# Performance work log

Hardware: AMD Instinct MI355X
Metric: run time of the kernel (lower is better)

The kernel has to match this reference:

```python
import jax, jax.numpy as jnp
import numpy as np
from jax import lax

H = W = 96
C = 3
N_PIX = H * W
N_PER_CLASS = 50   # min(size_sample_fg=100 -> shuffled to min_samples, size_sample_bg=50)
K = 5
THRESHOLD = 0.3
POS_WEIGHT = 100.0
CLEAN_THRESH = 0.6


def _sample_idx(key, valid_mask_flat, n):
    # Uniform random sample of n indices from valid positions (fixed-shape
    # replacement for tf.random.shuffle(tf.where(mask))[:n]).
    u = jax.random.uniform(key, (N_PIX,))
    score = jnp.where(valid_mask_flat, u, -1.0)
    _, idx = lax.top_k(score, n)
    return idx


def _pixel_features(img01):
    # img01: [H, W, C] in [0, 1]. Matches: reshape(img)/255 concat weighted positions.
    img_flat = img01.reshape(-1, C) / 255.0
    ii, jj = jnp.meshgrid(jnp.arange(H), jnp.arange(W), indexing='ij')
    pos = jnp.stack([ii, jj], axis=-1).reshape(-1, 2).astype(jnp.float32)
    pos = pos / jnp.array([H, W], jnp.float32) * POS_WEIGHT
    return jnp.concatenate([img_flat, pos], axis=1)  # [N_PIX, C+2]


def _process_image(img, key):
    # preprocess: (already 96x96x3) normalize & clip
    img_p = jnp.clip(img / 255.0, 0.0, 1.0)

    # extract_image_tf: clean image, pick fg/bg scribble pixels
    img_norm = img_p / jnp.max(img_p, axis=(0, 1), keepdims=True)
    cleaned = img_norm * (img_norm < CLEAN_THRESH).astype(jnp.float32)
    fg = jnp.any(cleaned > 0, axis=-1).reshape(-1)  # [N_PIX] bool
    bg = ~fg
    k_fg, k_bg = jax.random.split(key)
    fg_idx = _sample_idx(k_fg, fg, N_PER_CLASS)
    bg_idx = _sample_idx(k_bg, bg, N_PER_CLASS)

    # extract_features_tf
    feats_all = _pixel_features(img_p)                       # [N_PIX, 5]
    train_feats = jnp.concatenate([feats_all[fg_idx], feats_all[bg_idx]], axis=0)  # [100, 5]
    train_labels = jnp.concatenate([jnp.ones(N_PER_CLASS), jnp.zeros(N_PER_CLASS)])

    # segment_image_KNN_tf: standardize, brute-force cdist, top-k, label vote
    mean = jnp.mean(train_feats, axis=0)
    std = jnp.std(train_feats, axis=0)
    train_s = (train_feats - mean) / std                     # [100, 5]
    test_s = (feats_all - mean) / std                        # [N_PIX, 5]
    dist = jnp.sqrt(jnp.sum(jnp.square(test_s[:, None, :] - train_s[None, :, :]), axis=2))  # [N_PIX, 100]
    _, knn_idx = lax.top_k(-dist, K)                         # smallest-k distances
    probas = jnp.mean(train_labels[knn_idx], axis=1)         # [N_PIX]
    seg = (probas >= THRESHOLD).astype(jnp.int32).reshape(H, W)

    # mask original (preprocessed) image
    return jnp.where(seg[..., None] == 1, img_p, jnp.zeros_like(img_p))


def setup_inputs() -> dict:
    key = jax.random.key(0)
    images = jax.random.uniform(key, (32, H, W, C), dtype=jnp.float32)
    return {"images": images}


def reference(images):
    B = images.shape[0]
    keys = jax.random.split(jax.random.key(42), B)
    return jax.vmap(_process_image)(images, keys)
```

## Files before the change

### kernel.cpp

```cpp
#include <hip/hip_runtime.h>
#include <stdint.h>

#define NPIX 9216
#define NIMG 32
#define STRIP 1152

__device__ __forceinline__ uint32_t rotl32(uint32_t x, int d){ return (x<<d)|(x>>(32-d)); }

__device__ __forceinline__ void threefry(uint32_t k0, uint32_t k1, uint32_t x0, uint32_t x1,
                                         uint32_t &o0, uint32_t &o1){
  uint32_t ks2 = k0 ^ k1 ^ 0x1BD11BDAu;
  x0 += k0; x1 += k1;
  x0+=x1; x1=rotl32(x1,13); x1^=x0;
  x0+=x1; x1=rotl32(x1,15); x1^=x0;
  x0+=x1; x1=rotl32(x1,26); x1^=x0;
  x0+=x1; x1=rotl32(x1,6);  x1^=x0;
  x0+=k1; x1+=ks2+1u;
  x0+=x1; x1=rotl32(x1,17); x1^=x0;
  x0+=x1; x1=rotl32(x1,29); x1^=x0;
  x0+=x1; x1=rotl32(x1,16); x1^=x0;
  x0+=x1; x1=rotl32(x1,24); x1^=x0;
  x0+=ks2; x1+=k0+2u;
  x0+=x1; x1=rotl32(x1,13); x1^=x0;
  x0+=x1; x1=rotl32(x1,15); x1^=x0;
  x0+=x1; x1=rotl32(x1,26); x1^=x0;
  x0+=x1; x1=rotl32(x1,6);  x1^=x0;
  x0+=k0; x1+=k1+3u;
  x0+=x1; x1=rotl32(x1,17); x1^=x0;
  x0+=x1; x1=rotl32(x1,29); x1^=x0;
  x0+=x1; x1=rotl32(x1,16); x1^=x0;
  x0+=x1; x1=rotl32(x1,24); x1^=x0;
  x0+=k1; x1+=ks2+4u;
  x0+=x1; x1=rotl32(x1,13); x1^=x0;
  x0+=x1; x1=rotl32(x1,15); x1^=x0;
  x0+=x1; x1=rotl32(x1,26); x1^=x0;
  x0+=x1; x1=rotl32(x1,6);  x1^=x0;
  x0+=ks2; x1+=k0+5u;
  o0=x0; o1=x1;
}

__device__ __forceinline__ float clip01_div255(float x){
  return fminf(fmaxf(x/255.0f, 0.0f), 1.0f);
}

__global__ __launch_bounds__(256) void kmax(const float* __restrict__ in,
                                            float* __restrict__ maxpart){
  int img  = blockIdx.x / 6;
  int part = blockIdx.x % 6;
  int tid  = threadIdx.x;
  const float* base = in + (size_t)img*NPIX*3 + (size_t)part*1536*3;
  float m0=0.f, m1=0.f, m2=0.f;
#pragma unroll
  for(int k=0;k<18;k++){
    int g = k*256 + tid;
    float v = clip01_div255(base[g]);
    int c = g % 3;
    m0 = (c==0) ? fmaxf(m0,v) : m0;
    m1 = (c==1) ? fmaxf(m1,v) : m1;
    m2 = (c==2) ? fmaxf(m2,v) : m2;
  }
  for(int off=32; off>0; off>>=1){
    m0 = fmaxf(m0, __shfl_down(m0,off));
    m1 = fmaxf(m1, __shfl_down(m1,off));
    m2 = fmaxf(m2, __shfl_down(m2,off));
  }
  __shared__ float r[3][4];
  int lane = tid & 63, wv = tid >> 6;
  if(lane==0){ r[0][wv]=m0; r[1][wv]=m1; r[2][wv]=m2; }
  __syncthreads();
  if(tid==0){
    maxpart[blockIdx.x*3+0]=fmaxf(fmaxf(r[0][0],r[0][1]),fmaxf(r[0][2],r[0][3]));
    maxpart[blockIdx.x*3+1]=fmaxf(fmaxf(r[1][0],r[1][1]),fmaxf(r[1][2],r[1][3]));
    maxpart[blockIdx.x*3+2]=fmaxf(fmaxf(r[2][0],r[2][1]),fmaxf(r[2][2],r[2][3]));
  }
}

__global__ __launch_bounds__(256) void kscore(const float* __restrict__ in,
                                              const float* __restrict__ maxpart,
                                              unsigned long long* __restrict__ key50g){
#pragma clang fp contract(off)
  int b   = blockIdx.x;
  int img = b >> 4, cls = (b >> 3) & 1, sub = b & 7;
  int tid = threadIdx.x;

  __shared__ __attribute__((aligned(16))) float pixL[3456];
  __shared__ uint32_t vvL[STRIP];
  __shared__ uint64_t cand[STRIP];
  __shared__ int hist[129];
  __shared__ int ncand, bbin;

  if(tid<129) hist[tid]=0;
  if(tid==0)  ncand=0;

  const float* p = in + (size_t)img*NPIX*3;

  const float4* sp4 = (const float4*)(p + (size_t)sub*STRIP*3);
  float4* pixL4 = (float4*)pixL;
  for(int k=0;k<4;k++){ int i4=k*256+tid; if(i4<864) pixL4[i4]=sp4[i4]; }

  float c0=0.f,c1=0.f,c2=0.f;
#pragma unroll
  for(int s=0;s<6;s++){
    c0=fmaxf(c0, maxpart[(img*6+s)*3+0]);
    c1=fmaxf(c1, maxpart[(img*6+s)*3+1]);
    c2=fmaxf(c2, maxpart[(img*6+s)*3+2]);
  }

  uint32_t ik0, ik1; threefry(0u, 42u, 0u, (uint32_t)img, ik0, ik1);
  uint32_t s0, s1;   threefry(ik0, ik1, 0u, (uint32_t)cls, s0, s1);
  __syncthreads();

  for(int r=0;r<5;r++){
    int pi = tid + r*256;
    if(pi<STRIP){
      float a  = clip01_div255(pixL[pi*3+0])/c0;
      float bb = clip01_div255(pixL[pi*3+1])/c1;
      float c  = clip01_div255(pixL[pi*3+2])/c2;
      bool fg = (a>0.f && a<0.6f) || (bb>0.f && bb<0.6f) || (c>0.f && c<0.6f);
      bool valid = (cls==0) ? fg : !fg;
      uint32_t gi = (uint32_t)(sub*STRIP + pi);
      uint32_t r1,r2; threefry(s0, s1, 0u, gi, r1, r2);
      uint32_t vv = valid ? ((r1 ^ r2) >> 9) + 1u : 0u;
      vvL[pi] = vv;
      if(vv) atomicAdd(&hist[vv>>16], 1);
    }
  }
  __syncthreads();

  if(tid < 64){
    int h0 = hist[2*tid];
    int h1 = hist[2*tid+1];
    int h128 = hist[128];
    int S = h0 + h1;
    for(int off=1; off<64; off<<=1){
      int o = __shfl_down(S, off);
      if(tid + off < 64) S += o;
    }
    int ss0 = S + h128;
    int ss1 = S - h0 + h128;
    int cd = -1;
    if(ss0 >= 50) cd = 2*tid;
    if(ss1 >= 50) cd = 2*tid+1;
    if(tid==63 && h128 >= 50) cd = 128;
    for(int off=32; off>0; off>>=1){
      int o = __shfl_down(cd, off);
      cd = o > cd ? o : cd;
    }
    if(tid==0) bbin = cd;
  }
  __syncthreads();

  int bb = bbin;
  for(int r=0;r<5;r++){
    int pi = tid + r*256;
    if(pi<STRIP){
      uint32_t vv = vvL[pi];
      if((int)(vv>>16) >= bb){
        int pos = atomicAdd(&ncand,1);
        cand[pos] = ((uint64_t)vv << 14) | (uint64_t)(16383 - (sub*STRIP + pi));
      }
    }
  }
  __syncthreads();
  int m = ncand;
  for(int c=tid;c<m;c+=256){
    uint64_t k = cand[c];
    int r = 0, j = 0;
    while(j < m){
      int je = j+64 < m ? j+64 : m;
      for(; j<je; j++) r += (cand[j] > k);
      if(r >= 50) break;
    }
    if(r < 50) key50g[(size_t)b*50 + r] = k;
  }
}

__global__ __launch_bounds__(256) void kmerge(const float* __restrict__ in,
                                              const unsigned long long* __restrict__ key50g,
                                              float* __restrict__ ts2g,
                                              float* __restrict__ meanstd){
#pragma clang fp contract(off)
  int img = blockIdx.x;
  int tid = threadIdx.x;
  __shared__ uint64_t kk[800];
  __shared__ int      tIdx[100];
  __shared__ float    feat[100][5];
  __shared__ float    mv[5], sv[5];

  const uint64_t* kg = (const uint64_t*)key50g + (size_t)img*800;
  for(int c=tid;c<800;c+=256) kk[c] = kg[c];
  __syncthreads();

  for(int c=tid;c<800;c+=256){
    uint64_t k = kk[c];
    int cl = (c >= 400);
    int base = cl*400;
    int r = 0;
#pragma unroll
    for(int s=0;s<8;s++){
      const uint64_t* L = &kk[base + s*50];
      int lo=0, hi=50;
      while(lo<hi){ int mid=(lo+hi)>>1; if(L[mid] > k) lo=mid+1; else hi=mid; }
      r += lo;
    }
    if(r < 50) tIdx[cl*50+r] = 16383 - (int)(k & 16383u);
  }
  __syncthreads();

  if(tid<100){
    int pp = tIdx[tid];
    int i=pp/96, j=pp-i*96;
    const float* px = in + ((size_t)img*NPIX + pp)*3;
    for(int c=0;c<3;c++){
      float ip=clip01_div255(px[c]);
      feat[tid][c]=ip/255.0f;
    }
    feat[tid][3]=((float)i/96.0f)*100.0f;
    feat[tid][4]=((float)j/96.0f)*100.0f;
  }
  __syncthreads();
  if(tid<5){
    float s=0.f;
    for(int r=0;r<100;r++) s=s+feat[r][tid];
    float mu=s/100.0f; mv[tid]=mu;
    float v=0.f;
    for(int r=0;r<100;r++){ float d=feat[r][tid]-mu; float q=d*d; v=v+q; }
    sv[tid]=sqrtf(v/100.0f);
  }
  __syncthreads();
  if(tid<100){
    float r0=(feat[tid][0]-mv[0])/sv[0];
    float r1=(feat[tid][1]-mv[1])/sv[1];
    float r2=(feat[tid][2]-mv[2])/sv[2];
    float r3=(feat[tid][3]-mv[3])/sv[3];
    float r4=(feat[tid][4]-mv[4])/sv[4];
    float* dst = ts2g + img*600 + (tid>>1)*12 + (tid&1);
    dst[0]=r0; dst[2]=r1; dst[4]=r2; dst[6]=r3; dst[8]=r4;
  }
  if(tid<5)       meanstd[img*10+tid]=mv[tid];
  else if(tid<10) meanstd[img*10+tid]=sv[tid-5];
}

__global__ __launch_bounds__(256) void kknn(const float* __restrict__ in,
                                            const float* __restrict__ ts2g,
                                            const float* __restrict__ meanstd,
                                            float* __restrict__ out){
#pragma clang fp contract(off)
  int b     = blockIdx.x;
  int img   = b / 36;
  int chunk = b % 36;
  int tid   = threadIdx.x;

  __shared__ float    mv[5], sv[5];
  __shared__ __attribute__((aligned(16))) float ts2[600];
  __shared__ __attribute__((aligned(16))) float pix[768];

  if(tid<150) ((float4*)ts2)[tid] = ((const float4*)(ts2g + img*600))[tid];
  if(tid>=192 && tid<197) mv[tid-192]=meanstd[img*10+(tid-192)];
  if(tid>=224 && tid<229) sv[tid-224]=meanstd[img*10+5+(tid-224)];
  {
    const float4* cb4 = (const float4*)(in + ((size_t)img*NPIX + (size_t)chunk*256)*3);
    if(tid<192) ((float4*)pix)[tid] = cb4[tid];
  }
  __syncthreads();

  int p = chunk*256+tid;
  int i=p/96, j=p-i*96;
  float ip0=clip01_div255(pix[tid*3+0]);
  float ip1=clip01_div255(pix[tid*3+1]);
  float ip2=clip01_div255(pix[tid*3+2]);
  float t0,t1,t2,t3,t4;
  {
    float f0=ip0/255.0f, f1=ip1/255.0f, f2=ip2/255.0f;
    float f3=((float)i/96.0f)*100.0f, f4=((float)j/96.0f)*100.0f;
    t0=(f0-mv[0])/sv[0]; t1=(f1-mv[1])/sv[1]; t2=(f2-mv[2])/sv[2];
    t3=(f3-mv[3])/sv[3]; t4=(f4-mv[4])/sv[4];
  }

  float a0x=1e30f,a0y=1e30f, a1x=1e30f,a1y=1e30f;
#pragma unroll 5
  for(int pr=0;pr<25;pr++){
    const float* tp = &ts2[pr*12];
    float4 qA = *(const float4*)(tp);
    float4 qB = *(const float4*)(tp+4);
    float2 qC = *(const float2*)(tp+8);
    float sx, sy;
    { float dx=t0-qA.x, dy=t0-qA.y; sx=dx*dx; sy=dy*dy; }
    { float dx=t1-qA.z, dy=t1-qA.w; float wx=dx*dx, wy=dy*dy; sx=sx+wx; sy=sy+wy; }
    { float dx=t2-qB.x, dy=t2-qB.y; float wx=dx*dx, wy=dy*dy; sx=sx+wx; sy=sy+wy; }
    { float dx=t3-qB.z, dy=t3-qB.w; float wx=dx*dx, wy=dy*dy; sx=sx+wx; sy=sy+wy; }
    { float dx=t4-qC.x, dy=t4-qC.y; float wx=dx*dx, wy=dy*dy; sx=sx+wx; sy=sy+wy; }
    float tx=fmaxf(a0x,sx), ty=fmaxf(a0y,sy);
    a0x=fminf(a0x,sx);      a0y=fminf(a0y,sy);
    a1x=fminf(a1x,tx);      a1y=fminf(a1y,ty);
  }
  float a1 = fmaxf(fminf(a0x,a1y), fminf(a1x,a0y));

  float b0x=1e30f,b0y=1e30f, b1x=1e30f,b1y=1e30f;
  float b2x=1e30f,b2y=1e30f, b3x=1e30f,b3y=1e30f;
#pragma unroll 5
  for(int pr=25;pr<50;pr++){
    const float* tp = &ts2[pr*12];
    float4 qA = *(const float4*)(tp);
    float4 qB = *(const float4*)(tp+4);
    float2 qC = *(const float2*)(tp+8);
    float sx, sy;
    { float dx=t0-qA.x, dy=t0-qA.y; sx=dx*dx; sy=dy*dy; }
    { float dx=t1-qA.z, dy=t1-qA.w; float wx=dx*dx, wy=dy*dy; sx=sx+wx; sy=sy+wy; }
    { float dx=t2-qB.x, dy=t2-qB.y; float wx=dx*dx, wy=dy*dy; sx=sx+wx; sy=sy+wy; }
    { float dx=t3-qB.z, dy=t3-qB.w; float wx=dx*dx, wy=dy*dy; sx=sx+wx; sy=sy+wy; }
    { float dx=t4-qC.x, dy=t4-qC.y; float wx=dx*dx, wy=dy*dy; sx=sx+wx; sy=sy+wy; }
    float u0x=fmaxf(b0x,sx), u0y=fmaxf(b0y,sy);
    b0x=fminf(b0x,sx);       b0y=fminf(b0y,sy);
    float u1x=fmaxf(b1x,u0x), u1y=fmaxf(b1y,u0y);
    b1x=fminf(b1x,u0x);       b1y=fminf(b1y,u0y);
    float u2x=fmaxf(b2x,u1x), u2y=fmaxf(b2y,u1y);
    b2x=fminf(b2x,u1x);       b2y=fminf(b2y,u1y);
    b3x=fminf(b3x,u2x);       b3y=fminf(b3y,u2y);
  }
  float l0=fminf(b0x,b3y), l1=fminf(b1x,b2y), l2=fminf(b2x,b1y), l3=fminf(b3x,b0y);
  float b3 = fmaxf(fmaxf(l0,l1), fmaxf(l2,l3));

  bool seg = sqrtf(a1) <= sqrtf(b3);
  __syncthreads();
  pix[tid*3+0]=seg?ip0:0.f;
  pix[tid*3+1]=seg?ip1:0.f;
  pix[tid*3+2]=seg?ip2:0.f;
  __syncthreads();
  float4* ob4 = (float4*)(out + ((size_t)img*NPIX + (size_t)chunk*256)*3);
  if(tid<192) ob4[tid] = ((float4*)pix)[tid];
}

extern "C" void kernel_launch(void* const* d_in, const int* in_sizes, int n_in,
                              void* d_out, int out_size, void* d_ws, size_t ws_size,
                              hipStream_t stream) {
  const float* in = (const float*)d_in[0];
  float* out = (float*)d_out;
  float* maxpart = (float*)d_ws;
  unsigned long long* key50g = (unsigned long long*)((char*)d_ws + 2304);
  float* ts2g    = (float*)((char*)d_ws + 207104);
  float* meanstd = (float*)((char*)d_ws + 283904);

  kmax  <<<192,  256, 0, stream>>>(in, maxpart);
  kscore<<<512,  256, 0, stream>>>(in, maxpart, key50g);
  kmerge<<<32,   256, 0, stream>>>(in, key50g, ts2g, meanstd);
  kknn  <<<1152, 256, 0, stream>>>(in, ts2g, meanstd, out);
}
```

Baseline: 103.1 us.

## Fuse max and merge stages into neighbors, cutting four launches to two

```diff
diff --git a/kernel.cpp b/kernel.cpp
--- a/kernel.cpp
+++ b/kernel.cpp
@@ -43,43 +43,10 @@
   return fminf(fmaxf(x/255.0f, 0.0f), 1.0f);
 }
 
-__global__ __launch_bounds__(256) void kmax(const float* __restrict__ in,
-                                            float* __restrict__ maxpart){
-  int img  = blockIdx.x / 6;
-  int part = blockIdx.x % 6;
-  int tid  = threadIdx.x;
-  const float* base = in + (size_t)img*NPIX*3 + (size_t)part*1536*3;
-  float m0=0.f, m1=0.f, m2=0.f;
-#pragma unroll
-  for(int k=0;k<18;k++){
-    int g = k*256 + tid;
-    float v = clip01_div255(base[g]);
-    int c = g % 3;
-    m0 = (c==0) ? fmaxf(m0,v) : m0;
-    m1 = (c==1) ? fmaxf(m1,v) : m1;
-    m2 = (c==2) ? fmaxf(m2,v) : m2;
-  }
-  for(int off=32; off>0; off>>=1){
-    m0 = fmaxf(m0, __shfl_down(m0,off));
-    m1 = fmaxf(m1, __shfl_down(m1,off));
-    m2 = fmaxf(m2, __shfl_down(m2,off));
-  }
-  __shared__ float r[3][4];
-  int lane = tid & 63, wv = tid >> 6;
-  if(lane==0){ r[0][wv]=m0; r[1][wv]=m1; r[2][wv]=m2; }
-  __syncthreads();
-  if(tid==0){
-    maxpart[blockIdx.x*3+0]=fmaxf(fmaxf(r[0][0],r[0][1]),fmaxf(r[0][2],r[0][3]));
-    maxpart[blockIdx.x*3+1]=fmaxf(fmaxf(r[1][0],r[1][1]),fmaxf(r[1][2],r[1][3]));
-    maxpart[blockIdx.x*3+2]=fmaxf(fmaxf(r[2][0],r[2][1]),fmaxf(r[2][2],r[2][3]));
-  }
-}
-
 __global__ __launch_bounds__(256) void kscore(const float* __restrict__ in,
-                                              const float* __restrict__ maxpart,
                                               unsigned long long* __restrict__ key50g){
 #pragma clang fp contract(off)
-  int b   = blockIdx.x;
+  int b   = (blockIdx.x & 7)*64 + (blockIdx.x >> 3);
   int img = b >> 4, cls = (b >> 3) & 1, sub = b & 7;
   int tid = threadIdx.x;
 
@@ -88,6 +55,7 @@
   __shared__ uint64_t cand[STRIP];
   __shared__ int hist[129];
   __shared__ int ncand, bbin;
+  __shared__ float rmx[3][4];
 
   if(tid<129) hist[tid]=0;
   if(tid==0)  ncand=0;
@@ -98,17 +66,34 @@
   float4* pixL4 = (float4*)pixL;
   for(int k=0;k<4;k++){ int i4=k*256+tid; if(i4<864) pixL4[i4]=sp4[i4]; }
 
-  float c0=0.f,c1=0.f,c2=0.f;
-#pragma unroll
-  for(int s=0;s<6;s++){
-    c0=fmaxf(c0, maxpart[(img*6+s)*3+0]);
-    c1=fmaxf(c1, maxpart[(img*6+s)*3+1]);
-    c2=fmaxf(c2, maxpart[(img*6+s)*3+2]);
-  }
+  float m0=0.f, m1=0.f, m2=0.f;
+  const float4* ip4 = (const float4*)p;
+  for(int k=0;k<27;k++){
+    int i4 = k*256 + tid;
+    float4 v = ip4[i4];
+    float e0=clip01_div255(v.x), e1=clip01_div255(v.y),
+          e2=clip01_div255(v.z), e3=clip01_div255(v.w);
+    int b3 = i4 % 3;
+    float cb = fmaxf(e0,e3);
+    m0 = fmaxf(m0, b3==0 ? cb : (b3==1 ? e2 : e1));
+    m1 = fmaxf(m1, b3==0 ? e1 : (b3==1 ? cb : e2));
+    m2 = fmaxf(m2, b3==0 ? e2 : (b3==1 ? e1 : cb));
+  }
+  for(int off=32; off>0; off>>=1){
+    m0 = fmaxf(m0, __shfl_down(m0,off));
+    m1 = fmaxf(m1, __shfl_down(m1,off));
+    m2 = fmaxf(m2, __shfl_down(m2,off));
+  }
+  { int lane = tid & 63, wv = tid >> 6;
+    if(lane==0){ rmx[0][wv]=m0; rmx[1][wv]=m1; rmx[2][wv]=m2; } }
 
   uint32_t ik0, ik1; threefry(0u, 42u, 0u, (uint32_t)img, ik0, ik1);
   uint32_t s0, s1;   threefry(ik0, ik1, 0u, (uint32_t)cls, s0, s1);
   __syncthreads();
+
+  float c0 = fmaxf(fmaxf(rmx[0][0],rmx[0][1]), fmaxf(rmx[0][2],rmx[0][3]));
+  float c1 = fmaxf(fmaxf(rmx[1][0],rmx[1][1]), fmaxf(rmx[1][2],rmx[1][3]));
+  float c2 = fmaxf(fmaxf(rmx[2][0],rmx[2][1]), fmaxf(rmx[2][2],rmx[2][3]));
 
   for(int r=0;r<5;r++){
     int pi = tid + r*256;
@@ -175,20 +160,28 @@
   }
 }
 
-__global__ __launch_bounds__(256) void kmerge(const float* __restrict__ in,
-                                              const unsigned long long* __restrict__ key50g,
-                                              float* __restrict__ ts2g,
-                                              float* __restrict__ meanstd){
+__global__ __launch_bounds__(256) void kmknn(const float* __restrict__ in,
+                                             const unsigned long long* __restrict__ key50g,
+                                             float* __restrict__ out){
 #pragma clang fp contract(off)
-  int img = blockIdx.x;
-  int tid = threadIdx.x;
+  int b     = (blockIdx.x & 7)*144 + (blockIdx.x >> 3);
+  int img   = b / 36;
+  int chunk = b % 36;
+  int tid   = threadIdx.x;
+
   __shared__ uint64_t kk[800];
   __shared__ int      tIdx[100];
   __shared__ float    feat[100][5];
   __shared__ float    mv[5], sv[5];
+  __shared__ __attribute__((aligned(16))) float ts2[600];
+  __shared__ __attribute__((aligned(16))) float pix[768];
 
   const uint64_t* kg = (const uint64_t*)key50g + (size_t)img*800;
   for(int c=tid;c<800;c+=256) kk[c] = kg[c];
+  {
+    const float4* cb4 = (const float4*)(in + ((size_t)img*NPIX + (size_t)chunk*256)*3);
+    if(tid<192) ((float4*)pix)[tid] = cb4[tid];
+  }
   __syncthreads();
 
   for(int c=tid;c<800;c+=256){
@@ -234,33 +227,8 @@
     float r2=(feat[tid][2]-mv[2])/sv[2];
     float r3=(feat[tid][3]-mv[3])/sv[3];
     float r4=(feat[tid][4]-mv[4])/sv[4];
-    float* dst = ts2g + img*600 + (tid>>1)*12 + (tid&1);
+    float* dst = ts2 + (tid>>1)*12 + (tid&1);
     dst[0]=r0; dst[2]=r1; dst[4]=r2; dst[6]=r3; dst[8]=r4;
-  }
-  if(tid<5)       meanstd[img*10+tid]=mv[tid];
-  else if(tid<10) meanstd[img*10+tid]=sv[tid-5];
-}
-
-__global__ __launch_bounds__(256) void kknn(const float* __restrict__ in,
-                                            const float* __restrict__ ts2g,
-                                            const float* __restrict__ meanstd,
-                                            float* __restrict__ out){
-#pragma clang fp contract(off)
-  int b     = blockIdx.x;
-  int img   = b / 36;
-  int chunk = b % 36;
-  int tid   = threadIdx.x;
-
-  __shared__ float    mv[5], sv[5];
-  __shared__ __attribute__((aligned(16))) float ts2[600];
-  __shared__ __attribute__((aligned(16))) float pix[768];
-
-  if(tid<150) ((float4*)ts2)[tid] = ((const float4*)(ts2g + img*600))[tid];
-  if(tid>=192 && tid<197) mv[tid-192]=meanstd[img*10+(tid-192)];
-  if(tid>=224 && tid<229) sv[tid-224]=meanstd[img*10+5+(tid-224)];
-  {
-    const float4* cb4 = (const float4*)(in + ((size_t)img*NPIX + (size_t)chunk*256)*3);
-    if(tid<192) ((float4*)pix)[tid] = cb4[tid];
   }
   __syncthreads();
 
@@ -336,13 +304,8 @@
                               hipStream_t stream) {
   const float* in = (const float*)d_in[0];
   float* out = (float*)d_out;
-  float* maxpart = (float*)d_ws;
-  unsigned long long* key50g = (unsigned long long*)((char*)d_ws + 2304);
-  float* ts2g    = (float*)((char*)d_ws + 207104);
-  float* meanstd = (float*)((char*)d_ws + 283904);
-
-  kmax  <<<192,  256, 0, stream>>>(in, maxpart);
-  kscore<<<512,  256, 0, stream>>>(in, maxpart, key50g);
-  kmerge<<<32,   256, 0, stream>>>(in, key50g, ts2g, meanstd);
-  kknn  <<<1152, 256, 0, stream>>>(in, ts2g, meanstd, out);
-}
+  unsigned long long* key50g = (unsigned long long*)d_ws;
+
+  kscore<<<512,  256, 0, stream>>>(in, key50g);
+  kmknn <<<1152, 256, 0, stream>>>(in, key50g, out);
+}
```

After: 133.8 us. 29.8% more time.

## Fuse max, scoring, and top-50 selection into one per-image prep kernel

Applied to the files above, without the earlier changes.

```diff
diff --git a/kernel.cpp b/kernel.cpp
--- a/kernel.cpp
+++ b/kernel.cpp
@@ -3,7 +3,6 @@
 
 #define NPIX 9216
 #define NIMG 32
-#define STRIP 1152
 
 __device__ __forceinline__ uint32_t rotl32(uint32_t x, int d){ return (x<<d)|(x>>(32-d)); }
 
@@ -43,169 +42,134 @@
   return fminf(fmaxf(x/255.0f, 0.0f), 1.0f);
 }
 
-__global__ __launch_bounds__(256) void kmax(const float* __restrict__ in,
-                                            float* __restrict__ maxpart){
-  int img  = blockIdx.x / 6;
-  int part = blockIdx.x % 6;
-  int tid  = threadIdx.x;
-  const float* base = in + (size_t)img*NPIX*3 + (size_t)part*1536*3;
-  float m0=0.f, m1=0.f, m2=0.f;
-#pragma unroll
-  for(int k=0;k<18;k++){
-    int g = k*256 + tid;
-    float v = clip01_div255(base[g]);
-    int c = g % 3;
-    m0 = (c==0) ? fmaxf(m0,v) : m0;
-    m1 = (c==1) ? fmaxf(m1,v) : m1;
-    m2 = (c==2) ? fmaxf(m2,v) : m2;
-  }
-  for(int off=32; off>0; off>>=1){
-    m0 = fmaxf(m0, __shfl_down(m0,off));
-    m1 = fmaxf(m1, __shfl_down(m1,off));
-    m2 = fmaxf(m2, __shfl_down(m2,off));
-  }
-  __shared__ float r[3][4];
-  int lane = tid & 63, wv = tid >> 6;
-  if(lane==0){ r[0][wv]=m0; r[1][wv]=m1; r[2][wv]=m2; }
-  __syncthreads();
-  if(tid==0){
-    maxpart[blockIdx.x*3+0]=fmaxf(fmaxf(r[0][0],r[0][1]),fmaxf(r[0][2],r[0][3]));
-    maxpart[blockIdx.x*3+1]=fmaxf(fmaxf(r[1][0],r[1][1]),fmaxf(r[1][2],r[1][3]));
-    maxpart[blockIdx.x*3+2]=fmaxf(fmaxf(r[2][0],r[2][1]),fmaxf(r[2][2],r[2][3]));
-  }
-}
-
-__global__ __launch_bounds__(256) void kscore(const float* __restrict__ in,
-                                              const float* __restrict__ maxpart,
-                                              unsigned long long* __restrict__ key50g){
-#pragma clang fp contract(off)
-  int b   = blockIdx.x;
-  int img = b >> 4, cls = (b >> 3) & 1, sub = b & 7;
-  int tid = threadIdx.x;
-
-  __shared__ __attribute__((aligned(16))) float pixL[3456];
-  __shared__ uint32_t vvL[STRIP];
-  __shared__ uint64_t cand[STRIP];
-  __shared__ int hist[129];
-  __shared__ int ncand, bbin;
-
-  if(tid<129) hist[tid]=0;
-  if(tid==0)  ncand=0;
-
-  const float* p = in + (size_t)img*NPIX*3;
-
-  const float4* sp4 = (const float4*)(p + (size_t)sub*STRIP*3);
-  float4* pixL4 = (float4*)pixL;
-  for(int k=0;k<4;k++){ int i4=k*256+tid; if(i4<864) pixL4[i4]=sp4[i4]; }
-
-  float c0=0.f,c1=0.f,c2=0.f;
-#pragma unroll
-  for(int s=0;s<6;s++){
-    c0=fmaxf(c0, maxpart[(img*6+s)*3+0]);
-    c1=fmaxf(c1, maxpart[(img*6+s)*3+1]);
-    c2=fmaxf(c2, maxpart[(img*6+s)*3+2]);
-  }
-
-  uint32_t ik0, ik1; threefry(0u, 42u, 0u, (uint32_t)img, ik0, ik1);
-  uint32_t s0, s1;   threefry(ik0, ik1, 0u, (uint32_t)cls, s0, s1);
-  __syncthreads();
-
-  for(int r=0;r<5;r++){
-    int pi = tid + r*256;
-    if(pi<STRIP){
-      float a  = clip01_div255(pixL[pi*3+0])/c0;
-      float bb = clip01_div255(pixL[pi*3+1])/c1;
-      float c  = clip01_div255(pixL[pi*3+2])/c2;
-      bool fg = (a>0.f && a<0.6f) || (bb>0.f && bb<0.6f) || (c>0.f && c<0.6f);
-      bool valid = (cls==0) ? fg : !fg;
-      uint32_t gi = (uint32_t)(sub*STRIP + pi);
-      uint32_t r1,r2; threefry(s0, s1, 0u, gi, r1, r2);
-      uint32_t vv = valid ? ((r1 ^ r2) >> 9) + 1u : 0u;
-      vvL[pi] = vv;
-      if(vv) atomicAdd(&hist[vv>>16], 1);
-    }
-  }
-  __syncthreads();
-
-  if(tid < 64){
-    int h0 = hist[2*tid];
-    int h1 = hist[2*tid+1];
-    int h128 = hist[128];
-    int S = h0 + h1;
-    for(int off=1; off<64; off<<=1){
-      int o = __shfl_down(S, off);
-      if(tid + off < 64) S += o;
-    }
-    int ss0 = S + h128;
-    int ss1 = S - h0 + h128;
-    int cd = -1;
-    if(ss0 >= 50) cd = 2*tid;
-    if(ss1 >= 50) cd = 2*tid+1;
-    if(tid==63 && h128 >= 50) cd = 128;
-    for(int off=32; off>0; off>>=1){
-      int o = __shfl_down(cd, off);
-      cd = o > cd ? o : cd;
-    }
-    if(tid==0) bbin = cd;
-  }
-  __syncthreads();
-
-  int bb = bbin;
-  for(int r=0;r<5;r++){
-    int pi = tid + r*256;
-    if(pi<STRIP){
-      uint32_t vv = vvL[pi];
-      if((int)(vv>>16) >= bb){
-        int pos = atomicAdd(&ncand,1);
-        cand[pos] = ((uint64_t)vv << 14) | (uint64_t)(16383 - (sub*STRIP + pi));
-      }
-    }
-  }
-  __syncthreads();
-  int m = ncand;
-  for(int c=tid;c<m;c+=256){
-    uint64_t k = cand[c];
-    int r = 0, j = 0;
-    while(j < m){
-      int je = j+64 < m ? j+64 : m;
-      for(; j<je; j++) r += (cand[j] > k);
-      if(r >= 50) break;
-    }
-    if(r < 50) key50g[(size_t)b*50 + r] = k;
-  }
-}
-
-__global__ __launch_bounds__(256) void kmerge(const float* __restrict__ in,
-                                              const unsigned long long* __restrict__ key50g,
+__global__ __launch_bounds__(1024) void kprep(const float* __restrict__ in,
                                               float* __restrict__ ts2g,
                                               float* __restrict__ meanstd){
 #pragma clang fp contract(off)
   int img = blockIdx.x;
   int tid = threadIdx.x;
-  __shared__ uint64_t kk[800];
+
+  __shared__ uint32_t vvL[NPIX];
+  __shared__ uint64_t cand[2048];
+  __shared__ int      hist[2][129];
+  __shared__ int      nc, bbinL[2];
+  __shared__ float    cmaxL[3];
+  __shared__ float    wred[3][16];
   __shared__ int      tIdx[100];
   __shared__ float    feat[100][5];
   __shared__ float    mv[5], sv[5];
 
-  const uint64_t* kg = (const uint64_t*)key50g + (size_t)img*800;
-  for(int c=tid;c<800;c+=256) kk[c] = kg[c];
-  __syncthreads();
-
-  for(int c=tid;c<800;c+=256){
-    uint64_t k = kk[c];
-    int cl = (c >= 400);
-    int base = cl*400;
-    int r = 0;
-#pragma unroll
-    for(int s=0;s<8;s++){
-      const uint64_t* L = &kk[base + s*50];
-      int lo=0, hi=50;
-      while(lo<hi){ int mid=(lo+hi)>>1; if(L[mid] > k) lo=mid+1; else hi=mid; }
-      r += lo;
-    }
-    if(r < 50) tIdx[cl*50+r] = 16383 - (int)(k & 16383u);
-  }
-  __syncthreads();
+  if(tid<258) ((int*)hist)[tid]=0;
+
+  const float* p = in + (size_t)img*NPIX*3;
+
+  {
+    float m0=0.f, m1=0.f, m2=0.f;
+    for(int k=0;k<9;k++){
+      int px = k*1024 + tid;
+      m0 = fmaxf(m0, clip01_div255(p[px*3+0]));
+      m1 = fmaxf(m1, clip01_div255(p[px*3+1]));
+      m2 = fmaxf(m2, clip01_div255(p[px*3+2]));
+    }
+    for(int off=32; off>0; off>>=1){
+      m0 = fmaxf(m0, __shfl_down(m0,off));
+      m1 = fmaxf(m1, __shfl_down(m1,off));
+      m2 = fmaxf(m2, __shfl_down(m2,off));
+    }
+    int lane = tid & 63, wv = tid >> 6;
+    if(lane==0){ wred[0][wv]=m0; wred[1][wv]=m1; wred[2][wv]=m2; }
+  }
+  __syncthreads();
+  if(tid<3){
+    float m = wred[tid][0];
+    for(int w=1;w<16;w++) m = fmaxf(m, wred[tid][w]);
+    cmaxL[tid]=m;
+  }
+  __syncthreads();
+  float c0=cmaxL[0], c1=cmaxL[1], c2=cmaxL[2];
+
+  uint32_t ik0, ik1; threefry(0u, 42u, 0u, (uint32_t)img, ik0, ik1);
+  uint32_t sf0, sf1; threefry(ik0, ik1, 0u, 0u, sf0, sf1);
+  uint32_t sb0, sb1; threefry(ik0, ik1, 0u, 1u, sb0, sb1);
+
+  for(int k=0;k<9;k++){
+    int px = k*1024 + tid;
+    float a  = clip01_div255(p[px*3+0])/c0;
+    float bb = clip01_div255(p[px*3+1])/c1;
+    float c  = clip01_div255(p[px*3+2])/c2;
+    bool fg = (a>0.f && a<0.6f) || (bb>0.f && bb<0.6f) || (c>0.f && c<0.6f);
+    uint32_t k0 = fg ? sf0 : sb0, k1 = fg ? sf1 : sb1;
+    uint32_t r1, r2; threefry(k0, k1, 0u, (uint32_t)px, r1, r2);
+    uint32_t vv = ((r1 ^ r2) >> 9) + 1u;
+    vvL[px] = vv | (fg ? 0x80000000u : 0u);
+    atomicAdd(&hist[fg?0:1][vv>>16], 1);
+  }
+  __syncthreads();
+
+  if(tid<128){
+    int cls = tid>>6, l = tid&63;
+    int h0 = hist[cls][2*l];
+    int h1 = hist[cls][2*l+1];
+    int h128 = hist[cls][128];
+    int S = h0 + h1;
+    for(int off=1; off<64; off<<=1){
+      int o = __shfl_down(S, off);
+      if(l + off < 64) S += o;
+    }
+    int ss0 = S + h128;
+    int ss1 = S - h0 + h128;
+    int cd = -1;
+    if(ss0 >= 50) cd = 2*l;
+    if(ss1 >= 50) cd = 2*l+1;
+    if(l==63 && h128 >= 50) cd = 128;
+    for(int off=32; off>0; off>>=1){
+      int o = __shfl_down(cd, off);
+      cd = o > cd ? o : cd;
+    }
+    if(l==0) bbinL[cls] = cd;
+  }
+  __syncthreads();
+
+  for(int cls=0; cls<2; cls++){
+    if(tid==0) nc=0;
+    __syncthreads();
+    int bb = bbinL[cls];
+    uint32_t want = (cls==0) ? 0x80000000u : 0u;
+    for(int k=0;k<9;k++){
+      int px = k*1024 + tid;
+      uint32_t w = vvL[px];
+      if((w & 0x80000000u) == want){
+        uint32_t vv = w & 0x7FFFFFFFu;
+        if((int)(vv>>16) >= bb){
+          int pos = atomicAdd(&nc,1);
+          if(pos < 2048)
+            cand[pos] = ((uint64_t)vv << 14) | (uint64_t)(16383 - px);
+        }
+      }
+    }
+    __syncthreads();
+    int m = nc; if(m > 2048) m = 2048;
+    for(int c=tid; c<m; c+=1024){
+      uint64_t kk = cand[c];
+      int r = 0, j = 0;
+      while(j < m){
+        int je = j+64 < m ? j+64 : m;
+        for(; j<je; j++) r += (cand[j] > kk);
+        if(r >= 50) break;
+      }
+      if(r < 50) tIdx[cls*50 + r] = 16383 - (int)(kk & 16383u);
+    }
+    __syncthreads();
+    if(bb == -1){
+      if(tid==0){
+        int need = 50 - m, r = m;
+        for(int px=0; px<NPIX && need>0; px++){
+          if((vvL[px] & 0x80000000u) != want){ tIdx[cls*50 + r] = px; r++; need--; }
+        }
+      }
+      __syncthreads();
+    }
+  }
 
   if(tid<100){
     int pp = tIdx[tid];
@@ -336,13 +300,9 @@
                               hipStream_t stream) {
   const float* in = (const float*)d_in[0];
   float* out = (float*)d_out;
-  float* maxpart = (float*)d_ws;
-  unsigned long long* key50g = (unsigned long long*)((char*)d_ws + 2304);
-  float* ts2g    = (float*)((char*)d_ws + 207104);
-  float* meanstd = (float*)((char*)d_ws + 283904);
-
-  kmax  <<<192,  256, 0, stream>>>(in, maxpart);
-  kscore<<<512,  256, 0, stream>>>(in, maxpart, key50g);
-  kmerge<<<32,   256, 0, stream>>>(in, key50g, ts2g, meanstd);
-  kknn  <<<1152, 256, 0, stream>>>(in, ts2g, meanstd, out);
-}
+  float* ts2g    = (float*)d_ws;
+  float* meanstd = (float*)((char*)d_ws + 76800);
+
+  kprep<<<32,   1024, 0, stream>>>(in, ts2g, meanstd);
+  kknn <<<1152, 256,  0, stream>>>(in, ts2g, meanstd, out);
+}
```

Measured after the change: 117.6 us. +14.1%, slower.

## Merge fg and bg candidate selection into one kscore block per strip

Applied to the files above, without the earlier changes.

```diff
diff --git a/kernel.cpp b/kernel.cpp
--- a/kernel.cpp
+++ b/kernel.cpp
@@ -80,17 +80,17 @@
                                               unsigned long long* __restrict__ key50g){
 #pragma clang fp contract(off)
   int b   = blockIdx.x;
-  int img = b >> 4, cls = (b >> 3) & 1, sub = b & 7;
+  int img = b >> 3, sub = b & 7;
   int tid = threadIdx.x;
 
   __shared__ __attribute__((aligned(16))) float pixL[3456];
   __shared__ uint32_t vvL[STRIP];
-  __shared__ uint64_t cand[STRIP];
-  __shared__ int hist[129];
-  __shared__ int ncand, bbin;
-
-  if(tid<129) hist[tid]=0;
-  if(tid==0)  ncand=0;
+  __shared__ uint64_t cand[2][STRIP];
+  __shared__ int hist[258];
+  __shared__ int ncA[2], bbinL[2];
+
+  for(int i=tid;i<258;i+=256) hist[i]=0;
+  if(tid<2) ncA[tid]=0;
 
   const float* p = in + (size_t)img*NPIX*3;
 
@@ -107,7 +107,8 @@
   }
 
   uint32_t ik0, ik1; threefry(0u, 42u, 0u, (uint32_t)img, ik0, ik1);
-  uint32_t s0, s1;   threefry(ik0, ik1, 0u, (uint32_t)cls, s0, s1);
+  uint32_t sf0, sf1; threefry(ik0, ik1, 0u, 0u, sf0, sf1);
+  uint32_t sb0, sb1; threefry(ik0, ik1, 0u, 1u, sb0, sb1);
   __syncthreads();
 
   for(int r=0;r<5;r++){
@@ -117,61 +118,81 @@
       float bb = clip01_div255(pixL[pi*3+1])/c1;
       float c  = clip01_div255(pixL[pi*3+2])/c2;
       bool fg = (a>0.f && a<0.6f) || (bb>0.f && bb<0.6f) || (c>0.f && c<0.6f);
-      bool valid = (cls==0) ? fg : !fg;
+      uint32_t k0 = fg ? sf0 : sb0, k1 = fg ? sf1 : sb1;
       uint32_t gi = (uint32_t)(sub*STRIP + pi);
-      uint32_t r1,r2; threefry(s0, s1, 0u, gi, r1, r2);
-      uint32_t vv = valid ? ((r1 ^ r2) >> 9) + 1u : 0u;
-      vvL[pi] = vv;
-      if(vv) atomicAdd(&hist[vv>>16], 1);
-    }
-  }
-  __syncthreads();
-
-  if(tid < 64){
-    int h0 = hist[2*tid];
-    int h1 = hist[2*tid+1];
-    int h128 = hist[128];
+      uint32_t r1,r2; threefry(k0, k1, 0u, gi, r1, r2);
+      uint32_t vv = ((r1 ^ r2) >> 9) + 1u;
+      vvL[pi] = vv | (fg ? 0x80000000u : 0u);
+      atomicAdd(&hist[(fg?0:129) + (int)(vv>>16)], 1);
+    }
+  }
+  __syncthreads();
+
+  if(tid < 128){
+    int cls = tid>>6, l = tid&63;
+    int h0   = hist[cls*129 + 2*l];
+    int h1   = hist[cls*129 + 2*l+1];
+    int h128 = hist[cls*129 + 128];
     int S = h0 + h1;
     for(int off=1; off<64; off<<=1){
       int o = __shfl_down(S, off);
-      if(tid + off < 64) S += o;
+      if(l + off < 64) S += o;
     }
     int ss0 = S + h128;
     int ss1 = S - h0 + h128;
     int cd = -1;
-    if(ss0 >= 50) cd = 2*tid;
-    if(ss1 >= 50) cd = 2*tid+1;
-    if(tid==63 && h128 >= 50) cd = 128;
+    if(ss0 >= 50) cd = 2*l;
+    if(ss1 >= 50) cd = 2*l+1;
+    if(l==63 && h128 >= 50) cd = 128;
     for(int off=32; off>0; off>>=1){
       int o = __shfl_down(cd, off);
       cd = o > cd ? o : cd;
     }
-    if(tid==0) bbin = cd;
-  }
-  __syncthreads();
-
-  int bb = bbin;
-  for(int r=0;r<5;r++){
-    int pi = tid + r*256;
-    if(pi<STRIP){
-      uint32_t vv = vvL[pi];
-      if((int)(vv>>16) >= bb){
-        int pos = atomicAdd(&ncand,1);
-        cand[pos] = ((uint64_t)vv << 14) | (uint64_t)(16383 - (sub*STRIP + pi));
+    if(l==0) bbinL[cls] = cd;
+  }
+  __syncthreads();
+
+  {
+    int bb0 = bbinL[0], bb1 = bbinL[1];
+    for(int r=0;r<5;r++){
+      int pi = tid + r*256;
+      if(pi<STRIP){
+        uint32_t w  = vvL[pi];
+        int own     = (w & 0x80000000u) ? 0 : 1;
+        uint32_t vv = w & 0x7FFFFFFFu;
+        uint64_t tail = (uint64_t)(16383 - (sub*STRIP + pi));
+        int bbo = own ? bb1 : bb0;
+        if((int)(vv>>16) >= bbo){
+          int pos = atomicAdd(&ncA[own],1);
+          cand[own][pos] = ((uint64_t)vv << 14) | tail;
+        }
+        int bbt = own ? bb0 : bb1;
+        if(bbt == -1){
+          int oth = 1-own;
+          int pos = atomicAdd(&ncA[oth],1);
+          cand[oth][pos] = tail;
+        }
       }
     }
   }
   __syncthreads();
-  int m = ncand;
-  for(int c=tid;c<m;c+=256){
-    uint64_t k = cand[c];
-    int r = 0, j = 0;
-    while(j < m){
-      int je = j+64 < m ? j+64 : m;
-      for(; j<je; j++) r += (cand[j] > k);
-      if(r >= 50) break;
-    }
-    if(r < 50) key50g[(size_t)b*50 + r] = k;
+
+  {
+    int cls = (tid >= 128);
+    int lt  = tid & 127;
+    int m = ncA[cls];
+    const uint64_t* C = cand[cls];
+    unsigned long long* dst = key50g + (size_t)img*800 + (size_t)cls*400 + (size_t)sub*50;
+    for(int c=lt; c<m; c+=128){
+      uint64_t k = C[c];
+      int r = 0, j = 0;
+      while(j < m){
+        int je = j+64 < m ? j+64 : m;
+        for(; j<je; j++) r += (C[j] > k);
+        if(r >= 50) break;
+      }
+      if(r < 50) dst[r] = k;
+    }
   }
 }
 
@@ -342,7 +363,7 @@
   float* meanstd = (float*)((char*)d_ws + 283904);
 
   kmax  <<<192,  256, 0, stream>>>(in, maxpart);
-  kscore<<<512,  256, 0, stream>>>(in, maxpart, key50g);
+  kscore<<<256,  256, 0, stream>>>(in, maxpart, key50g);
   kmerge<<<32,   256, 0, stream>>>(in, key50g, ts2g, meanstd);
   kknn  <<<1152, 256, 0, stream>>>(in, ts2g, meanstd, out);
 }
```

Measured after the change: 103.3 us. No clear change (+0.2%).
